# Kernel tuning notes

Measured on AMD Instinct MI355X. Metric: run time of the kernel, lower is better.

Reference implementation:

```python
import jax, jax.numpy as jnp
import numpy as np

T, N = 1024, 128
V, H, VS, KS = 35, 512, 128, 128
MAX_LEN = 250


def setup_inputs() -> dict:
    key = jax.random.key(0)
    ks = jax.random.split(key, 16)
    s = 0.05
    emb = jax.random.normal(ks[0], (V, H), jnp.float32) * s
    emb = emb.at[0].set(0.0)  # padding_idx=0
    return {
        'enc_key': jax.random.normal(ks[1], (T, N, KS), jnp.float32),
        'enc_value': jax.random.normal(ks[2], (T, N, VS), jnp.float32),
        'lens': jax.random.randint(ks[3], (N,), 1, T, jnp.int32),
        'emb': emb,
        'W_ih1': jax.random.normal(ks[4], (4 * H, H + VS), jnp.float32) * s,
        'W_hh1': jax.random.normal(ks[5], (4 * H, H), jnp.float32) * s,
        'b_ih1': jax.random.normal(ks[6], (4 * H,), jnp.float32) * s,
        'b_hh1': jax.random.normal(ks[7], (4 * H,), jnp.float32) * s,
        'W_ih2': jax.random.normal(ks[8], (4 * KS, H), jnp.float32) * s,
        'W_hh2': jax.random.normal(ks[9], (4 * KS, KS), jnp.float32) * s,
        'b_ih2': jax.random.normal(ks[10], (4 * KS,), jnp.float32) * s,
        'b_hh2': jax.random.normal(ks[11], (4 * KS,), jnp.float32) * s,
        'W_out': jax.random.normal(ks[12], (V, KS + VS), jnp.float32) * s,
        'b_out': jax.random.normal(ks[13], (V,), jnp.float32) * s,
    }


def _lstm_cell(x, h, c, W_ih, W_hh, b_ih, b_hh):
    # PyTorch LSTMCell gate order: i, f, g, o
    g = x @ W_ih.T + b_ih + h @ W_hh.T + b_hh
    i, f, gg, o = jnp.split(g, 4, axis=-1)
    c_new = jax.nn.sigmoid(f) * c + jax.nn.sigmoid(i) * jnp.tanh(gg)
    h_new = jax.nn.sigmoid(o) * jnp.tanh(c_new)
    return h_new, c_new


def reference(enc_key, enc_value, lens, emb, W_ih1, W_hh1, b_ih1, b_hh1,
              W_ih2, W_hh2, b_ih2, b_hh2, W_out, b_out):
    # eval-mode forward (isTrain=False): greedy decode for MAX_LEN steps.
    key_t = jnp.transpose(enc_key, (1, 0, 2))    # (N, T, KS)
    val_t = jnp.transpose(enc_value, (1, 0, 2))  # (N, T, VS)
    values_mean = enc_value.mean(axis=0)         # (N, VS) -- fed to lstm1 every step (as in source)
    mask = jnp.arange(T)[None, :] >= lens[:, None]  # (N, T) True = masked

    h1 = jnp.zeros((N, H), enc_key.dtype)
    c1 = jnp.zeros((N, H), enc_key.dtype)
    h2 = jnp.zeros((N, KS), enc_key.dtype)
    c2 = jnp.zeros((N, KS), enc_key.dtype)
    tok0 = jnp.zeros((N,), jnp.int32)  # argmax of ones(N,1)*33 over size-1 dim == 0

    def step(carry, _):
        h1, c1, h2, c2, tok = carry
        char_embed = emb[tok]                                  # (N, H)
        inp = jnp.concatenate([char_embed, values_mean], axis=1)
        h1n, c1n = _lstm_cell(inp, h1, c1, W_ih1, W_hh1, b_ih1, b_hh1)
        h2n, c2n = _lstm_cell(h1n, h2, c2, W_ih2, W_hh2, b_ih2, b_hh2)
        energy = jnp.einsum('ntk,nk->nt', key_t, h2n)          # (N, T)
        energy = jnp.where(mask, -1e9, energy)
        attn = jax.nn.softmax(energy, axis=1)
        ctx = jnp.einsum('nt,ntv->nv', attn, val_t)            # (N, VS)
        pred = jnp.concatenate([h2n, ctx], axis=1) @ W_out.T + b_out  # (N, V)
        tok_n = jnp.argmax(pred, axis=-1).astype(jnp.int32)
        return (h1n, c1n, h2n, c2n, tok_n), pred

    _, preds = jax.lax.scan(step, (h1, c1, h2, c2, tok0), None, length=MAX_LEN)
    return jnp.transpose(preds, (1, 0, 2))  # (N, MAX_LEN, V)
```

## Files before the change

### kernel.cpp

```cpp
#include <hip/hip_runtime.h>
#include <math.h>

typedef unsigned int u32;
typedef unsigned long long ull;
typedef float f4v __attribute__((ext_vector_type(4)));

#define T_     1024
#define N_     128
#define V_     35
#define H_     512
#define VS_    128
#define KS_    128
#define MAXLEN 250
#define NBLK   256

#define OFF_TOKF   0
#define OFF_H1F    512
#define OFF_H2OF   1536
#define OFF_H2HF   2048
#define OFF_PFLAG  2560
#define OFF_PMS    3072
#define OFF_H2P    4096
#define OFF_PCTX   69632
#define OFF_VM     135168
#define OFF_EMBG   200704
#define OFF_VMG    487424
#define OFF_H1A    1536000
#define OFF_H1B    1798144
#define OFF_W1P    2060288
#define OFF_W2TO   6254592
#define OFF_W2TH   6909952
#define OFF_B2O    7565312
#define OFF_B2H    7566336
#define OFF_WO2    7567360
#define OFF_KT     8388608ull
#define OFF_VT     75497472ull
#define WS_T_NEED  142606336ull

#define ASF_STR 516
#define WSBUF   4352

__device__ __forceinline__ float sigf(float x){ return 1.0f/(1.0f+expf(-x)); }
__device__ __forceinline__ float dot4(float4 a, float4 b){ return a.x*b.x + a.y*b.y + a.z*b.z + a.w*b.w; }

__device__ __forceinline__ float cohloadf(const float* p){
  return __hip_atomic_load(p, __ATOMIC_RELAXED, __HIP_MEMORY_SCOPE_AGENT);
}
__device__ __forceinline__ void cohstoref(float* p, float v){
  __hip_atomic_store(p, v, __ATOMIC_RELAXED, __HIP_MEMORY_SCOPE_AGENT);
}
__device__ __forceinline__ ull cohloadu(const ull* p){
  return __hip_atomic_load(p, __ATOMIC_RELAXED, __HIP_MEMORY_SCOPE_AGENT);
}
__device__ __forceinline__ u32 cohloadw(const u32* p){
  return __hip_atomic_load(p, __ATOMIC_RELAXED, __HIP_MEMORY_SCOPE_AGENT);
}
__device__ __forceinline__ void cohstorew(u32* p, u32 v){
  __hip_atomic_store(p, v, __ATOMIC_RELAXED, __HIP_MEMORY_SCOPE_AGENT);
}

__global__ void prep_state(const float* __restrict__ val, char* __restrict__ ws){
  __shared__ float part[256];
  float* vmarr = (float*)(ws + OFF_VM);
  float* h1A   = (float*)(ws + OFF_H1A);
  const int n = blockIdx.x, tid = threadIdx.x;
  const int c = tid >> 7, v = tid & 127;
  float acc = 0.f;
  const float* vp = val + (size_t)(c*512)*N_*VS_ + (size_t)n*VS_ + v;
  #pragma unroll 8
  for (int t = 0; t < 512; ++t) acc += vp[(size_t)t*N_*VS_];
  part[tid] = acc;
  __syncthreads();
  if (tid < 128) vmarr[(size_t)n*128 + tid] = (part[tid] + part[tid+128]) * (1.0f/1024.0f);
  h1A[(size_t)n*H_ + tid]       = 0.f;
  h1A[(size_t)n*H_ + 256 + tid] = 0.f;
}

__global__ void prep_embG(const float* __restrict__ emb, const float* __restrict__ W_ih1,
                          char* __restrict__ ws){
  float* embG = (float*)(ws + OFF_EMBG);
  const int v = blockIdx.x >> 3, cb = blockIdx.x & 7;
  const int c = cb*256 + threadIdx.x;
  const int row_w = (c & 3)*H_ + (c >> 2);
  const float4* w4 = (const float4*)(W_ih1 + (size_t)row_w*640);
  const float4* e4 = (const float4*)(emb + (size_t)v*H_);
  float s = 0.f;
  #pragma unroll 8
  for (int k = 0; k < 128; ++k) s += dot4(w4[k], e4[k]);
  embG[(size_t)v*2048 + c] = s;
}

__global__ void prep_vmG(const float* __restrict__ W_ih1, const float* __restrict__ b_ih1,
                         const float* __restrict__ b_hh1, char* __restrict__ ws){
  float* vmG = (float*)(ws + OFF_VMG);
  const float* vmarr = (const float*)(ws + OFF_VM);
  const int n = blockIdx.x >> 3, cb = blockIdx.x & 7;
  const int c = cb*256 + threadIdx.x;
  const int row_w = (c & 3)*H_ + (c >> 2);
  const float4* w4 = (const float4*)(W_ih1 + (size_t)row_w*640 + 512);
  const float4* v4 = (const float4*)(vmarr + (size_t)n*128);
  float s = b_ih1[row_w] + b_hh1[row_w];
  #pragma unroll 8
  for (int k = 0; k < 32; ++k) s += dot4(w4[k], v4[k]);
  vmG[(size_t)n*2048 + c] = s;
}

__global__ void prep_W1p(const float* __restrict__ W_hh1, char* __restrict__ ws){
  float* Wp1 = (float*)(ws + OFF_W1P);
  const int ct = blockIdx.x >> 3, ch = blockIdx.x & 7, tid = threadIdx.x;
  const int c_st = tid >> 2, seg = tid & 3;
  const int sgl = ct*64 + c_st, row_w = (sgl & 3)*H_ + (sgl >> 2);
  const float* src = W_hh1 + (size_t)row_w*H_ + ch*64 + seg*16;
  float* dstb = Wp1 + (size_t)ct*32768 + ch*4096 + tid*4;
  #pragma unroll
  for (int j = 0; j < 4; ++j)
    *(float4*)(dstb + j*1024) = *(const float4*)(src + j*4);
}

__global__ void prep_W2T(const float* __restrict__ W_ih2, const float* __restrict__ W_hh2,
                         const float* __restrict__ b_ih2, const float* __restrict__ b_hh2,
                         char* __restrict__ ws){
  float* W2To = (float*)(ws + OFF_W2TO);
  float* W2Th = (float*)(ws + OFF_W2TH);
  const int k = blockIdx.x, tid = threadIdx.x;
  const int g = tid >> 6, uu = tid & 63;
  const int rowO = g*128 + uu, rowH = g*128 + 64 + uu;
  float vo, vh;
  if (k < 512){ vo = W_ih2[(size_t)rowO*512 + k]; vh = W_ih2[(size_t)rowH*512 + k]; }
  else        { vo = W_hh2[(size_t)rowO*128 + (k-512)]; vh = W_hh2[(size_t)rowH*128 + (k-512)]; }
  W2To[(size_t)k*256 + tid] = vo;
  W2Th[(size_t)k*256 + tid] = vh;
  if (k == 0){
    ((float*)(ws + OFF_B2O))[tid] = b_ih2[rowO] + b_hh2[rowO];
    ((float*)(ws + OFF_B2H))[tid] = b_ih2[rowH] + b_hh2[rowH];
  }
}

__global__ void prep_Wo2(const float* __restrict__ W_out, char* __restrict__ ws){
  float* Wo2 = (float*)(ws + OFF_WO2);
  const int idx = blockIdx.x*256 + threadIdx.x;
  const int k = idx >> 6, v = idx & 63;
  Wo2[idx] = (v < V_) ? W_out[(size_t)v*256 + k] : 0.f;
}

__global__ void prep_transpose(const float* __restrict__ key, const float* __restrict__ val,
                               char* __restrict__ ws){
  float* keyT = (float*)(ws + OFF_KT);
  float* valT = (float*)(ws + OFF_VT);
  const int bt = blockIdx.x & 1023;
  const bool isv = blockIdx.x >= 1024;
  const float* src = isv ? val : key;
  float* dst = isv ? valT : keyT;
  const int nn = threadIdx.x >> 1, hf = threadIdx.x & 1;
  const float4* s4 = (const float4*)(src + ((size_t)bt*N_ + nn)*KS_ + hf*64);
  float4* d4 = (float4*)(dst + ((size_t)nn*T_ + bt)*KS_ + hf*64);
  #pragma unroll
  for (int i = 0; i < 16; ++i) d4[i] = s4[i];
}

__global__ __launch_bounds__(256, 1) void decoder_main(
  const float* __restrict__ keyA, const float* __restrict__ valA,
  const ull nstr, const ull kstr,
  const int* __restrict__ lens, const float* __restrict__ b_out,
  float* __restrict__ out, char* __restrict__ ws)
{
  __shared__ __align__(16) float smem[16*ASF_STR + 2*WSBUF];
  __shared__ float c1_keep[256];
  __shared__ float h2_keep[128];
  __shared__ float c2_keep[64];
  __shared__ int   toksh[16];

  float* AsF = smem;
  float* WsB = smem + 16*ASF_STR;

  u32* tokflag = (u32*)(ws + OFF_TOKF);
  u32* h1flag  = (u32*)(ws + OFF_H1F);
  u32* h2of    = (u32*)(ws + OFF_H2OF);
  u32* h2hf    = (u32*)(ws + OFF_H2HF);
  u32* pflag   = (u32*)(ws + OFF_PFLAG);
  float* pms   = (float*)(ws + OFF_PMS);
  float* h2p   = (float*)(ws + OFF_H2P);
  float* pctx  = (float*)(ws + OFF_PCTX);
  float* embG  = (float*)(ws + OFF_EMBG);
  float* vmG   = (float*)(ws + OFF_VMG);
  float* h1cur = (float*)(ws + OFF_H1A);
  float* h1nxt = (float*)(ws + OFF_H1B);
  const float* Wp1 = (const float*)(ws + OFF_W1P);
  const float* Wo2 = (const float*)(ws + OFF_WO2);

  const int b = blockIdx.x, tid = threadIdx.x;

  c1_keep[tid] = 0.f;
  if (tid < 128) h2_keep[tid] = 0.f;
  if (tid < 64)  c2_keep[tid] = 0.f;

  const int rt = b >> 5, ct = b & 31;
  const int row0 = rt*16, c0 = ct*64;
  const int lane = tid & 63, qw = tid >> 6;
  const int r_g = lane >> 4, c_g = lane & 15;
  const int c_st = tid >> 2, seg = tid & 3;
  const float* wct = Wp1 + (size_t)ct*32768 + (tid << 2);

  const int n = b & 127;
  const bool owner = (b < 128);
  const float* W2T = (const float*)(ws + (owner ? OFF_W2TO : OFF_W2TH));
  const float* b2  = (const float*)(ws + (owner ? OFF_B2O : OFF_B2H));
  const int len = lens[n];
  const int mid = (7*len) >> 4;
  const int lo = owner ? 0 : mid;
  const int hi = owner ? mid : len;
  const float* krow = keyA + (size_t)n*nstr;
  const float* vrow = valA + (size_t)n*nstr;

  float* xs   = smem;
  float* ctxL = smem + 640;
  float* G2p  = smem + 640;
  float* G2   = smem + 1664;
  float* h2s  = smem + 1920;
  float* Es   = smem + 2048;
  float* red  = smem + 3072;
  float* Cs   = smem + 3136;
  float* Zs   = smem + 4160;
  float* Prp  = smem + 4416;

  #pragma unroll 1
  for (int step = 0; step < MAXLEN; ++step){
    {
      float4 w0 = *(const float4*)(wct),
             w1 = *(const float4*)(wct+1024),
             w2 = *(const float4*)(wct+2048),
             w3 = *(const float4*)(wct+3072);

      if (tid < 16){
        u32 tv;
        const u32 tgt = (u32)step << 8;
        while ((tv = cohloadw(&tokflag[row0 + tid])) < tgt) __builtin_amdgcn_s_sleep(1);
        toksh[tid] = (int)(tv & 255u);
      }
      __syncthreads();

      {
        const ull* src = (const ull*)(h1cur + (size_t)row0*H_);
        ull* dstb = (ull*)AsF;
        #pragma unroll
        for (int i = 0; i < 16; ++i){
          const int u = tid + i*256;
          const int r = u >> 8, cc = u & 255;
          dstb[(size_t)r*258 + cc] = cohloadu(src + u);
        }
      }

      float acc[4][4];
      #pragma unroll
      for (int i = 0; i < 4; ++i){ acc[i][0]=0.f; acc[i][1]=0.f; acc[i][2]=0.f; acc[i][3]=0.f; }

      #pragma unroll 1
      for (int ch = 0; ch < 8; ++ch){
        float* W = WsB + (ch & 1)*WSBUF;
        { float* wd = W + c_st*68 + seg*16;
          ((float4*)wd)[0]=w0; ((float4*)wd)[1]=w1; ((float4*)wd)[2]=w2; ((float4*)wd)[3]=w3;
        }
        if (ch < 7){
          const float* q = wct + (ch+1)*4096;
          w0 = *(const float4*)(q);      w1 = *(const float4*)(q+1024);
          w2 = *(const float4*)(q+2048); w3 = *(const float4*)(q+3072);
        }
        __syncthreads();
        const int kbase = ch*64;
        #pragma unroll
        for (int kq = 0; kq < 4; ++kq){
          const int t4 = (qw*4 + kq)*4;
          float4 wv0 = *(const float4*)(W + (c_g   )*68 + t4);
          float4 wv1 = *(const float4*)(W + (c_g+16)*68 + t4);
          float4 wv2 = *(const float4*)(W + (c_g+32)*68 + t4);
          float4 wv3 = *(const float4*)(W + (c_g+48)*68 + t4);
          const int ko = kbase + t4;
          float4 av0 = *(const float4*)(AsF + (r_g   )*ASF_STR + ko);
          float4 av1 = *(const float4*)(AsF + (r_g+ 4)*ASF_STR + ko);
          float4 av2 = *(const float4*)(AsF + (r_g+ 8)*ASF_STR + ko);
          float4 av3 = *(const float4*)(AsF + (r_g+12)*ASF_STR + ko);
          acc[0][0]+=dot4(av0,wv0); acc[0][1]+=dot4(av0,wv1); acc[0][2]+=dot4(av0,wv2); acc[0][3]+=dot4(av0,wv3);
          acc[1][0]+=dot4(av1,wv0); acc[1][1]+=dot4(av1,wv1); acc[1][2]+=dot4(av1,wv2); acc[1][3]+=dot4(av1,wv3);
          acc[2][0]+=dot4(av2,wv0); acc[2][1]+=dot4(av2,wv1); acc[2][2]+=dot4(av2,wv2); acc[2][3]+=dot4(av2,wv3);
          acc[3][0]+=dot4(av3,wv0); acc[3][1]+=dot4(av3,wv1); acc[3][2]+=dot4(av3,wv2); acc[3][3]+=dot4(av3,wv3);
        }
        __syncthreads();
      }
      float* Red = WsB;
      #pragma unroll
      for (int ri = 0; ri < 4; ++ri)
        #pragma unroll
        for (int ci = 0; ci < 4; ++ci)
          Red[((ri*4+ci)*4 + qw)*64 + lane] = acc[ri][ci];
      __syncthreads();
      float* Gs = AsF;
      { const int l2 = tid & 63, g = tid >> 6;
        const int row_l = (l2 >> 4) + 4*g;
        const int nrow = row0 + row_l;
        const float* eg = embG + (size_t)toksh[row_l]*2048 + c0;
        const float* vg = vmG  + (size_t)nrow*2048 + c0;
        #pragma unroll
        for (int j = 0; j < 4; ++j){
          const int a = g*4 + j;
          const float* rp = Red + a*256 + l2;
          float s = rp[0] + rp[64] + rp[128] + rp[192];
          const int col_l = (l2 & 15) + 16*j;
          s += eg[col_l] + vg[col_l];
          Gs[row_l*68 + col_l] = s;
        }
      }
      __syncthreads();
      { const int r = tid >> 4, hl = tid & 15;
        float4 q = *(const float4*)(Gs + r*68 + hl*4);
        const int row = row0 + r, hid = ct*16 + hl;
        float cold = c1_keep[tid];
        float cn = sigf(q.y)*cold + sigf(q.x)*tanhf(q.z);
        float hn = sigf(q.w)*tanhf(cn);
        c1_keep[tid] = cn;
        cohstoref(h1nxt + (size_t)row*H_ + hid, hn);
      }
      __syncthreads();
      if (tid == 0) cohstorew(&h1flag[rt*32 + ct], (u32)(step+1));
    }

    {
      if (tid < 32){
        while (cohloadw(&h1flag[(n >> 4)*32 + tid]) < (u32)(step+1)) __builtin_amdgcn_s_sleep(1);
      }
      __syncthreads();
      xs[tid]       = cohloadf(h1nxt + (size_t)n*H_ + tid);
      xs[256 + tid] = cohloadf(h1nxt + (size_t)n*H_ + 256 + tid);
      if (tid < 128) xs[512 + tid] = h2_keep[tid];
      __syncthreads();

      {
        const int kw = tid >> 6, cl = tid & 63;
        const float* Wt = W2T + (size_t)kw*160*256 + cl*4;
        const float* xk = xs + kw*160;
        f4v acc = {0.f,0.f,0.f,0.f};
        #pragma unroll 4
        for (int k = 0; k < 160; ++k)
          acc += xk[k] * *(const f4v*)(Wt + (size_t)k*256);
        ((f4v*)(G2p + kw*256))[cl] = acc;
      }
      __syncthreads();
      G2[tid] = G2p[tid] + G2p[256+tid] + G2p[512+tid] + G2p[768+tid] + b2[tid];
      __syncthreads();
      if (tid < 64){
        const int unit = owner ? tid : (64 + tid);
        float gi = G2[tid], gf = G2[64+tid], gg = G2[128+tid], go = G2[192+tid];
        float cold = c2_keep[tid];
        float cn = sigf(gf)*cold + sigf(gi)*tanhf(gg);
        float hn = sigf(go)*tanhf(cn);
        c2_keep[tid] = cn;
        cohstoref(h2p + (size_t)n*128 + unit, hn);
      }
      __syncthreads();
      if (tid == 0){
        cohstorew(owner ? &h2of[n] : &h2hf[n], (u32)(step+1));
        u32* of = owner ? &h2hf[n] : &h2of[n];
        while (cohloadw(of) < (u32)(step+1)) __builtin_amdgcn_s_sleep(1);
      }
      __syncthreads();
      if (tid < 128){
        float hv = cohloadf(h2p + (size_t)n*128 + tid);
        h2s[tid] = hv; h2_keep[tid] = hv;
      }
      __syncthreads();
    }

    {
      const float4* h2f = (const float4*)h2s;
      const int grp = tid >> 4, gj = tid & 15;
      const float4 hq0 = h2f[gj*2], hq1 = h2f[gj*2+1];
      for (int t = lo + grp; t < hi; t += 16){
        const float4* kp = (const float4*)(krow + (size_t)t*kstr + gj*8);
        float e = dot4(kp[0], hq0) + dot4(kp[1], hq1);
        e += __shfl_xor(e, 1); e += __shfl_xor(e, 2);
        e += __shfl_xor(e, 4); e += __shfl_xor(e, 8);
        if (gj == 0) Es[t] = e;
      }
      __syncthreads();
      float lm = -3.0e38f;
      for (int t = lo + tid; t < hi; t += 256) lm = fmaxf(lm, Es[t]);
      #pragma unroll
      for (int off = 32; off > 0; off >>= 1) lm = fmaxf(lm, __shfl_xor(lm, off));
      if (lane == 0) red[qw] = lm;
      __syncthreads();
      const float m_l = fmaxf(fmaxf(red[0], red[1]), fmaxf(red[2], red[3]));
      __syncthreads();
      float ls = 0.f;
      for (int t = lo + tid; t < hi; t += 256){ float p = expf(Es[t]-m_l); Es[t] = p; ls += p; }
      #pragma unroll
      for (int off = 32; off > 0; off >>= 1) ls += __shfl_xor(ls, off);
      if (lane == 0) red[qw] = ls;
      __syncthreads();
      const float s_l = red[0] + red[1] + red[2] + red[3];
      { const int part = tid >> 5, v4i = (tid & 31)*4;
        f4v a0 = {0.f,0.f,0.f,0.f}, a1 = a0, a2 = a0, a3 = a0;
        int t = lo + part;
        for (; t + 24 < hi; t += 32){
          float p0 = Es[t], p1 = Es[t+8], p2 = Es[t+16], p3 = Es[t+24];
          f4v u0 = *(const f4v*)(vrow + (size_t)(t    )*kstr + v4i);
          f4v u1 = *(const f4v*)(vrow + (size_t)(t+ 8 )*kstr + v4i);
          f4v u2 = *(const f4v*)(vrow + (size_t)(t+16 )*kstr + v4i);
          f4v u3 = *(const f4v*)(vrow + (size_t)(t+24 )*kstr + v4i);
          a0 += p0*u0; a1 += p1*u1; a2 += p2*u2; a3 += p3*u3;
        }
        for (; t < hi; t += 8){
          f4v u0 = *(const f4v*)(vrow + (size_t)t*kstr + v4i);
          a0 += Es[t]*u0;
        }
        f4v ctv = a0 + a1 + a2 + a3;
        Cs[part*128 + v4i+0]=ctv.x; Cs[part*128 + v4i+1]=ctv.y;
        Cs[part*128 + v4i+2]=ctv.z; Cs[part*128 + v4i+3]=ctv.w;
      }
      __syncthreads();
      if (tid < 128){
        float s = 0.f;
        #pragma unroll
        for (int p8 = 0; p8 < 8; ++p8) s += Cs[p8*128 + tid];
        ctxL[tid] = s;
      }
      __syncthreads();

      if (!owner){
        if (tid < 128) cohstoref(pctx + (size_t)n*128 + tid, ctxL[tid]);
        if (tid == 0){ cohstoref(pms + 2*n, m_l); cohstoref(pms + 2*n + 1, s_l); }
        __syncthreads();
        if (tid == 0) cohstorew(&pflag[n], (u32)(step+1));
      } else {
        if (tid == 0){
          while (cohloadw(&pflag[n]) < (u32)(step+1)) __builtin_amdgcn_s_sleep(1);
        }
        __syncthreads();
        if (tid < 128){
          float m2 = cohloadf(pms + 2*n), s2v = cohloadf(pms + 2*n + 1);
          float c2v = cohloadf(pctx + (size_t)n*128 + tid);
          float m = fmaxf(m_l, m2);
          float e1 = expf(m_l - m), e2 = expf(m2 - m);
          float denom = e1*s_l + e2*s2v;
          Zs[tid]       = h2s[tid];
          Zs[128 + tid] = (e1*ctxL[tid] + e2*c2v) / denom;
        }
        __syncthreads();
        {
          const int kw = tid >> 6, lv = tid & 63;
          const float* wp = Wo2 + (size_t)kw*64*64 + lv;
          const float* zk = Zs + kw*64;
          float a = 0.f;
          #pragma unroll 8
          for (int k = 0; k < 64; ++k) a += zk[k]*wp[(size_t)k*64];
          Prp[kw*64 + lv] = a;
        }
        __syncthreads();
        if (tid < 64){
          float s = Prp[tid] + Prp[64+tid] + Prp[128+tid] + Prp[192+tid];
          float av = (tid < V_) ? (s + b_out[tid]) : -3.0e38f;
          if (tid < V_) out[((size_t)n*MAXLEN + step)*V_ + tid] = av;
          float bv = av; int bi = tid;
          #pragma unroll
          for (int off = 32; off > 0; off >>= 1){
            float ov = __shfl_xor(bv, off);
            int   oi = __shfl_xor(bi, off);
            if (ov > bv || (ov == bv && oi < bi)){ bv = ov; bi = oi; }
          }
          if (tid == 0) cohstorew(&tokflag[n], ((u32)(step+1) << 8) | (u32)bi);
        }
      }
    }
    __syncthreads();
    float* tp = h1cur; h1cur = h1nxt; h1nxt = tp;
  }
}

extern "C" void kernel_launch(void* const* d_in, const int* in_sizes, int n_in,
                              void* d_out, int out_size, void* d_ws, size_t ws_size,
                              hipStream_t stream)
{
  const float* key    = (const float*)d_in[0];
  const float* val    = (const float*)d_in[1];
  const int*   lens   = (const int*)d_in[2];
  const float* emb    = (const float*)d_in[3];
  const float* W_ih1  = (const float*)d_in[4];
  const float* W_hh1  = (const float*)d_in[5];
  const float* b_ih1  = (const float*)d_in[6];
  const float* b_hh1  = (const float*)d_in[7];
  const float* W_ih2  = (const float*)d_in[8];
  const float* W_hh2  = (const float*)d_in[9];
  const float* b_ih2  = (const float*)d_in[10];
  const float* b_hh2  = (const float*)d_in[11];
  const float* W_out  = (const float*)d_in[12];
  const float* b_out  = (const float*)d_in[13];

  (void)in_sizes; (void)n_in; (void)out_size;

  (void)hipMemsetAsync(d_ws, 0, 4096, stream);
  prep_state<<<128, 256, 0, stream>>>(val, (char*)d_ws);
  prep_embG<<<280, 256, 0, stream>>>(emb, W_ih1, (char*)d_ws);
  prep_vmG<<<1024, 256, 0, stream>>>(W_ih1, b_ih1, b_hh1, (char*)d_ws);
  prep_W1p<<<256, 256, 0, stream>>>(W_hh1, (char*)d_ws);
  prep_W2T<<<640, 256, 0, stream>>>(W_ih2, W_hh2, b_ih2, b_hh2, (char*)d_ws);
  prep_Wo2<<<64, 256, 0, stream>>>(W_out, (char*)d_ws);

  const int use_t = (ws_size >= WS_T_NEED) ? 1 : 0;
  const float* keyA = key; const float* valA = val;
  ull nstr = (ull)KS_, kstr = (ull)N_*KS_;
  if (use_t){
    prep_transpose<<<2048, 256, 0, stream>>>(key, val, (char*)d_ws);
    keyA = (const float*)((char*)d_ws + OFF_KT);
    valA = (const float*)((char*)d_ws + OFF_VT);
    nstr = (ull)T_*KS_; kstr = (ull)KS_;
  }

  decoder_main<<<NBLK, 256, 0, stream>>>(
      keyA, valA, nstr, kstr, lens, b_out,
      (float*)d_out, (char*)d_ws);
}
```

Before: 14.41 ms.

## Split attention over four blocks per sequence when occupancy allows two blocks per CU

When the occupancy query reports at least two resident blocks per CU, the persistent decoder launches 512 blocks instead of 256. Each sequence's time axis is then split into four chunks: 256 extra blocks handle only attention and wait on the h2 flags. The owner block merges three partial softmax/context results instead of one, and the energy loop is unrolled by two. The aim is to spread the memory-bound key/value attention across more CUs and shorten each step's critical path. The cost is more flag polling and merge work, and the spin-wait scheme only works if all 512 blocks are actually co-resident.

```diff
diff --git a/kernel.cpp b/kernel.cpp
--- a/kernel.cpp
+++ b/kernel.cpp
@@ -12,27 +12,26 @@
 #define VS_    128
 #define KS_    128
 #define MAXLEN 250
-#define NBLK   256
 
 #define OFF_TOKF   0
 #define OFF_H1F    512
 #define OFF_H2OF   1536
 #define OFF_H2HF   2048
 #define OFF_PFLAG  2560
-#define OFF_PMS    3072
-#define OFF_H2P    4096
-#define OFF_PCTX   69632
-#define OFF_VM     135168
-#define OFF_EMBG   200704
-#define OFF_VMG    487424
-#define OFF_H1A    1536000
-#define OFF_H1B    1798144
-#define OFF_W1P    2060288
-#define OFF_W2TO   6254592
-#define OFF_W2TH   6909952
-#define OFF_B2O    7565312
-#define OFF_B2H    7566336
-#define OFF_WO2    7567360
+#define OFF_PMS    4096
+#define OFF_H2P    8192
+#define OFF_PCTX   73728
+#define OFF_VM     270336
+#define OFF_EMBG   335872
+#define OFF_VMG    622592
+#define OFF_H1A    1671168
+#define OFF_H1B    1933312
+#define OFF_W1P    2195456
+#define OFF_W2TO   6389760
+#define OFF_W2TH   7045120
+#define OFF_B2O    7700480
+#define OFF_B2H    7701504
+#define OFF_WO2    7702528
 #define OFF_KT     8388608ull
 #define OFF_VT     75497472ull
 #define WS_T_NEED  142606336ull
@@ -160,7 +159,7 @@
 
 __global__ __launch_bounds__(256, 1) void decoder_main(
   const float* __restrict__ keyA, const float* __restrict__ valA,
-  const ull nstr, const ull kstr,
+  const ull nstr, const ull kstr, const int nsplit,
   const int* __restrict__ lens, const float* __restrict__ b_out,
   float* __restrict__ out, char* __restrict__ ws)
 {
@@ -189,26 +188,35 @@
   const float* Wo2 = (const float*)(ws + OFF_WO2);
 
   const int b = blockIdx.x, tid = threadIdx.x;
+  const int roleIdx = b >> 7;
+  const int n = b & 127;
+  const bool owner = (roleIdx == 0);
+  const bool isAB  = (b < 256);
 
   c1_keep[tid] = 0.f;
   if (tid < 128) h2_keep[tid] = 0.f;
   if (tid < 64)  c2_keep[tid] = 0.f;
 
   const int rt = b >> 5, ct = b & 31;
-  const int row0 = rt*16, c0 = ct*64;
+  const int row0 = (rt & 7)*16, c0 = ct*64;
   const int lane = tid & 63, qw = tid >> 6;
   const int r_g = lane >> 4, c_g = lane & 15;
   const int c_st = tid >> 2, seg = tid & 3;
   const float* wct = Wp1 + (size_t)ct*32768 + (tid << 2);
 
-  const int n = b & 127;
-  const bool owner = (b < 128);
   const float* W2T = (const float*)(ws + (owner ? OFF_W2TO : OFF_W2TH));
   const float* b2  = (const float*)(ws + (owner ? OFF_B2O : OFF_B2H));
   const int len = lens[n];
-  const int mid = (7*len) >> 4;
-  const int lo = owner ? 0 : mid;
-  const int hi = owner ? mid : len;
+  int w0i, w1i;
+  if (nsplit == 4){
+    w0i = (roleIdx==0) ? 0 : (roleIdx==1) ? 6 : (roleIdx==2) ? 15 : 24;
+    w1i = (roleIdx==0) ? 6 : (roleIdx==1) ? 15 : (roleIdx==2) ? 24 : 32;
+  } else {
+    w0i = (roleIdx==0) ? 0 : 14;
+    w1i = (roleIdx==0) ? 14 : 32;
+  }
+  const int lo = (len*w0i) >> 5;
+  const int hi = (len*w1i) >> 5;
   const float* krow = keyA + (size_t)n*nstr;
   const float* vrow = valA + (size_t)n*nstr;
 
@@ -225,7 +233,7 @@
 
   #pragma unroll 1
   for (int step = 0; step < MAXLEN; ++step){
-    {
+    if (isAB){
       float4 w0 = *(const float4*)(wct),
              w1 = *(const float4*)(wct+1024),
              w2 = *(const float4*)(wct+2048),
@@ -320,10 +328,10 @@
         cohstoref(h1nxt + (size_t)row*H_ + hid, hn);
       }
       __syncthreads();
-      if (tid == 0) cohstorew(&h1flag[rt*32 + ct], (u32)(step+1));
+      if (tid == 0) cohstorew(&h1flag[(rt & 7)*32 + ct], (u32)(step+1));
     }
 
-    {
+    if (isAB){
       if (tid < 32){
         while (cohloadw(&h1flag[(n >> 4)*32 + tid]) < (u32)(step+1)) __builtin_amdgcn_s_sleep(1);
       }
@@ -367,13 +375,34 @@
         h2s[tid] = hv; h2_keep[tid] = hv;
       }
       __syncthreads();
+    } else {
+      if (tid == 0){
+        while (cohloadw(&h2of[n]) < (u32)(step+1)) __builtin_amdgcn_s_sleep(1);
+        while (cohloadw(&h2hf[n]) < (u32)(step+1)) __builtin_amdgcn_s_sleep(1);
+      }
+      __syncthreads();
+      if (tid < 128) h2s[tid] = cohloadf(h2p + (size_t)n*128 + tid);
+      __syncthreads();
     }
 
     {
       const float4* h2f = (const float4*)h2s;
       const int grp = tid >> 4, gj = tid & 15;
       const float4 hq0 = h2f[gj*2], hq1 = h2f[gj*2+1];
-      for (int t = lo + grp; t < hi; t += 16){
+      int t = lo + grp;
+      for (; t + 16 < hi; t += 32){
+        const float4* kp0 = (const float4*)(krow + (size_t)t*kstr + gj*8);
+        const float4* kp1 = (const float4*)(krow + (size_t)(t+16)*kstr + gj*8);
+        float4 a0 = kp0[0], a1 = kp0[1], b0v = kp1[0], b1v = kp1[1];
+        float e0 = dot4(a0,hq0) + dot4(a1,hq1);
+        float e1 = dot4(b0v,hq0) + dot4(b1v,hq1);
+        e0 += __shfl_xor(e0, 1); e1 += __shfl_xor(e1, 1);
+        e0 += __shfl_xor(e0, 2); e1 += __shfl_xor(e1, 2);
+        e0 += __shfl_xor(e0, 4); e1 += __shfl_xor(e1, 4);
+        e0 += __shfl_xor(e0, 8); e1 += __shfl_xor(e1, 8);
+        if (gj == 0){ Es[t] = e0; Es[t+16] = e1; }
+      }
+      for (; t < hi; t += 16){
         const float4* kp = (const float4*)(krow + (size_t)t*kstr + gj*8);
         float e = dot4(kp[0], hq0) + dot4(kp[1], hq1);
         e += __shfl_xor(e, 1); e += __shfl_xor(e, 2);
@@ -382,7 +411,7 @@
       }
       __syncthreads();
       float lm = -3.0e38f;
-      for (int t = lo + tid; t < hi; t += 256) lm = fmaxf(lm, Es[t]);
+      for (int tt = lo + tid; tt < hi; tt += 256) lm = fmaxf(lm, Es[tt]);
       #pragma unroll
       for (int off = 32; off > 0; off >>= 1) lm = fmaxf(lm, __shfl_xor(lm, off));
       if (lane == 0) red[qw] = lm;
@@ -390,7 +419,7 @@
       const float m_l = fmaxf(fmaxf(red[0], red[1]), fmaxf(red[2], red[3]));
       __syncthreads();
       float ls = 0.f;
-      for (int t = lo + tid; t < hi; t += 256){ float p = expf(Es[t]-m_l); Es[t] = p; ls += p; }
+      for (int tt = lo + tid; tt < hi; tt += 256){ float p = expf(Es[tt]-m_l); Es[tt] = p; ls += p; }
       #pragma unroll
       for (int off = 32; off > 0; off >>= 1) ls += __shfl_xor(ls, off);
       if (lane == 0) red[qw] = ls;
@@ -398,18 +427,18 @@
       const float s_l = red[0] + red[1] + red[2] + red[3];
       { const int part = tid >> 5, v4i = (tid & 31)*4;
         f4v a0 = {0.f,0.f,0.f,0.f}, a1 = a0, a2 = a0, a3 = a0;
-        int t = lo + part;
-        for (; t + 24 < hi; t += 32){
-          float p0 = Es[t], p1 = Es[t+8], p2 = Es[t+16], p3 = Es[t+24];
-          f4v u0 = *(const f4v*)(vrow + (size_t)(t    )*kstr + v4i);
-          f4v u1 = *(const f4v*)(vrow + (size_t)(t+ 8 )*kstr + v4i);
-          f4v u2 = *(const f4v*)(vrow + (size_t)(t+16 )*kstr + v4i);
-          f4v u3 = *(const f4v*)(vrow + (size_t)(t+24 )*kstr + v4i);
+        int tc = lo + part;
+        for (; tc + 24 < hi; tc += 32){
+          float p0 = Es[tc], p1 = Es[tc+8], p2 = Es[tc+16], p3 = Es[tc+24];
+          f4v u0 = *(const f4v*)(vrow + (size_t)(tc    )*kstr + v4i);
+          f4v u1 = *(const f4v*)(vrow + (size_t)(tc+ 8 )*kstr + v4i);
+          f4v u2 = *(const f4v*)(vrow + (size_t)(tc+16 )*kstr + v4i);
+          f4v u3 = *(const f4v*)(vrow + (size_t)(tc+24 )*kstr + v4i);
           a0 += p0*u0; a1 += p1*u1; a2 += p2*u2; a3 += p3*u3;
         }
-        for (; t < hi; t += 8){
-          f4v u0 = *(const f4v*)(vrow + (size_t)t*kstr + v4i);
-          a0 += Es[t]*u0;
+        for (; tc < hi; tc += 8){
+          f4v u0 = *(const f4v*)(vrow + (size_t)tc*kstr + v4i);
+          a0 += Es[tc]*u0;
         }
         f4v ctv = a0 + a1 + a2 + a3;
         Cs[part*128 + v4i+0]=ctv.x; Cs[part*128 + v4i+1]=ctv.y;
@@ -424,24 +453,35 @@
       }
       __syncthreads();
 
-      if (!owner){
-        if (tid < 128) cohstoref(pctx + (size_t)n*128 + tid, ctxL[tid]);
-        if (tid == 0){ cohstoref(pms + 2*n, m_l); cohstoref(pms + 2*n + 1, s_l); }
+      if (roleIdx != 0){
+        const int hs = roleIdx - 1;
+        if (tid < 128) cohstoref(pctx + (size_t)hs*16384 + (size_t)n*128 + tid, ctxL[tid]);
+        if (tid == 0){ cohstoref(pms + hs*256 + 2*n, m_l); cohstoref(pms + hs*256 + 2*n + 1, s_l); }
         __syncthreads();
-        if (tid == 0) cohstorew(&pflag[n], (u32)(step+1));
+        if (tid == 0) cohstorew(&pflag[hs*128 + n], (u32)(step+1));
       } else {
         if (tid == 0){
-          while (cohloadw(&pflag[n]) < (u32)(step+1)) __builtin_amdgcn_s_sleep(1);
+          for (int hs = 0; hs < nsplit-1; ++hs){
+            while (cohloadw(&pflag[hs*128 + n]) < (u32)(step+1)) __builtin_amdgcn_s_sleep(1);
+          }
         }
         __syncthreads();
         if (tid < 128){
-          float m2 = cohloadf(pms + 2*n), s2v = cohloadf(pms + 2*n + 1);
-          float c2v = cohloadf(pctx + (size_t)n*128 + tid);
-          float m = fmaxf(m_l, m2);
-          float e1 = expf(m_l - m), e2 = expf(m2 - m);
-          float denom = e1*s_l + e2*s2v;
+          float m = m_l;
+          for (int hs = 0; hs < nsplit-1; ++hs)
+            m = fmaxf(m, cohloadf(pms + hs*256 + 2*n));
+          float e0 = expf(m_l - m);
+          float denom = e0*s_l;
+          float cacc  = e0*ctxL[tid];
+          for (int hs = 0; hs < nsplit-1; ++hs){
+            float mh = cohloadf(pms + hs*256 + 2*n);
+            float sh = cohloadf(pms + hs*256 + 2*n + 1);
+            float ch = cohloadf(pctx + (size_t)hs*16384 + (size_t)n*128 + tid);
+            float e = expf(mh - m);
+            denom += e*sh; cacc += e*ch;
+          }
           Zs[tid]       = h2s[tid];
-          Zs[128 + tid] = (e1*ctxL[tid] + e2*c2v) / denom;
+          Zs[128 + tid] = cacc / denom;
         }
         __syncthreads();
         {
@@ -495,7 +535,7 @@
 
   (void)in_sizes; (void)n_in; (void)out_size;
 
-  (void)hipMemsetAsync(d_ws, 0, 4096, stream);
+  (void)hipMemsetAsync(d_ws, 0, 8192, stream);
   prep_state<<<128, 256, 0, stream>>>(val, (char*)d_ws);
   prep_embG<<<280, 256, 0, stream>>>(emb, W_ih1, (char*)d_ws);
   prep_vmG<<<1024, 256, 0, stream>>>(W_ih1, b_ih1, b_hh1, (char*)d_ws);
@@ -513,7 +553,12 @@
     nstr = (ull)T_*KS_; kstr = (ull)KS_;
   }
 
-  decoder_main<<<NBLK, 256, 0, stream>>>(
-      keyA, valA, nstr, kstr, lens, b_out,
+  int maxb = 0;
+  (void)hipOccupancyMaxActiveBlocksPerMultiprocessor(&maxb, decoder_main, 256, 0);
+  const int nsplit = (maxb >= 2) ? 4 : 2;
+  const int grid   = (nsplit == 4) ? 512 : 256;
+
+  decoder_main<<<grid, 256, 0, stream>>>(
+      keyA, valA, nstr, kstr, nsplit, lens, b_out,
       (float*)d_out, (char*)d_ws);
 }
```

Result: faster. 12.61 ms (-12.5%).

## Add helper prefetch blocks that warm key/value rows into cache each step

Applied to the files above, without the earlier changes.

Launches an extra 256 blocks when occupancy allows two blocks per CU. The helper blocks spin on the per-sequence token flag and then stream that sequence's key and value rows, keeping them resident in cache (L2/MALL) for the attention pass of the compute blocks. Workspace offsets are shifted to make room, and the host queries device and function attributes to decide the grid size. The helpers add memory traffic and contend for CU resources. If co-residency does not hold, they rely on a bounded spin to avoid deadlock.

```diff
diff --git a/kernel.cpp b/kernel.cpp
--- a/kernel.cpp
+++ b/kernel.cpp
@@ -1,5 +1,6 @@
 #include <hip/hip_runtime.h>
 #include <math.h>
+#include <string.h>
 
 typedef unsigned int u32;
 typedef unsigned long long ull;
@@ -12,27 +13,26 @@
 #define VS_    128
 #define KS_    128
 #define MAXLEN 250
-#define NBLK   256
 
 #define OFF_TOKF   0
 #define OFF_H1F    512
 #define OFF_H2OF   1536
 #define OFF_H2HF   2048
 #define OFF_PFLAG  2560
-#define OFF_PMS    3072
-#define OFF_H2P    4096
-#define OFF_PCTX   69632
-#define OFF_VM     135168
-#define OFF_EMBG   200704
-#define OFF_VMG    487424
-#define OFF_H1A    1536000
-#define OFF_H1B    1798144
-#define OFF_W1P    2060288
-#define OFF_W2TO   6254592
-#define OFF_W2TH   6909952
-#define OFF_B2O    7565312
-#define OFF_B2H    7566336
-#define OFF_WO2    7567360
+#define OFF_PMS    4096
+#define OFF_H2P    8192
+#define OFF_PCTX   73728
+#define OFF_VM     270336
+#define OFF_EMBG   335872
+#define OFF_VMG    622592
+#define OFF_H1A    1671168
+#define OFF_H1B    1933312
+#define OFF_W1P    2195456
+#define OFF_W2TO   6389760
+#define OFF_W2TH   7045120
+#define OFF_B2O    7700480
+#define OFF_B2H    7701504
+#define OFF_WO2    7702528
 #define OFF_KT     8388608ull
 #define OFF_VT     75497472ull
 #define WS_T_NEED  142606336ull
@@ -170,10 +170,45 @@
   __shared__ float c2_keep[64];
   __shared__ int   toksh[16];
 
+  u32* tokflag = (u32*)(ws + OFF_TOKF);
+
+  const int b = blockIdx.x, tid = threadIdx.x;
+
+  if (b >= 256){
+    const int n2   = b & 127;
+    const int half = ((b >> 7) == 2) ? 0 : 1;
+    const int len2 = lens[n2];
+    const int mid2 = (7*len2) >> 4;
+    const int plo  = half ? mid2 : 0;
+    const int phi  = half ? len2 : mid2;
+    const float* kr = keyA + (size_t)n2*nstr;
+    const float* vr = valA + (size_t)n2*nstr;
+    const int rown = tid >> 3;
+    const int segi = (tid & 7) * 4;
+    f4v sink = {0.f,0.f,0.f,0.f};
+    for (int step = 0; step < MAXLEN; ++step){
+      const u32 tgt = (u32)step << 8;
+      int sp = 0;
+      while (cohloadw(&tokflag[n2]) < tgt){
+        __builtin_amdgcn_s_sleep(16);
+        if (++sp > (1<<19)) break;
+      }
+      for (int t = plo + rown; t < phi; t += 32){
+        const f4v* kp = (const f4v*)(kr + (size_t)t*kstr) + segi;
+        sink += kp[0]; sink += kp[1]; sink += kp[2]; sink += kp[3];
+      }
+      for (int t = plo + rown; t < phi; t += 32){
+        const f4v* vp = (const f4v*)(vr + (size_t)t*kstr) + segi;
+        sink += vp[0]; sink += vp[1]; sink += vp[2]; sink += vp[3];
+      }
+    }
+    asm volatile("" :: "v"(sink[0]), "v"(sink[1]), "v"(sink[2]), "v"(sink[3]));
+    return;
+  }
+
   float* AsF = smem;
   float* WsB = smem + 16*ASF_STR;
 
-  u32* tokflag = (u32*)(ws + OFF_TOKF);
   u32* h1flag  = (u32*)(ws + OFF_H1F);
   u32* h2of    = (u32*)(ws + OFF_H2OF);
   u32* h2hf    = (u32*)(ws + OFF_H2HF);
@@ -187,8 +222,6 @@
   float* h1nxt = (float*)(ws + OFF_H1B);
   const float* Wp1 = (const float*)(ws + OFF_W1P);
   const float* Wo2 = (const float*)(ws + OFF_WO2);
-
-  const int b = blockIdx.x, tid = threadIdx.x;
 
   c1_keep[tid] = 0.f;
   if (tid < 128) h2_keep[tid] = 0.f;
@@ -382,7 +415,7 @@
       }
       __syncthreads();
       float lm = -3.0e38f;
-      for (int t = lo + tid; t < hi; t += 256) lm = fmaxf(lm, Es[t]);
+      for (int tt = lo + tid; tt < hi; tt += 256) lm = fmaxf(lm, Es[tt]);
       #pragma unroll
       for (int off = 32; off > 0; off >>= 1) lm = fmaxf(lm, __shfl_xor(lm, off));
       if (lane == 0) red[qw] = lm;
@@ -390,7 +423,7 @@
       const float m_l = fmaxf(fmaxf(red[0], red[1]), fmaxf(red[2], red[3]));
       __syncthreads();
       float ls = 0.f;
-      for (int t = lo + tid; t < hi; t += 256){ float p = expf(Es[t]-m_l); Es[t] = p; ls += p; }
+      for (int tt = lo + tid; tt < hi; tt += 256){ float p = expf(Es[tt]-m_l); Es[tt] = p; ls += p; }
       #pragma unroll
       for (int off = 32; off > 0; off >>= 1) ls += __shfl_xor(ls, off);
       if (lane == 0) red[qw] = ls;
@@ -398,18 +431,18 @@
       const float s_l = red[0] + red[1] + red[2] + red[3];
       { const int part = tid >> 5, v4i = (tid & 31)*4;
         f4v a0 = {0.f,0.f,0.f,0.f}, a1 = a0, a2 = a0, a3 = a0;
-        int t = lo + part;
-        for (; t + 24 < hi; t += 32){
-          float p0 = Es[t], p1 = Es[t+8], p2 = Es[t+16], p3 = Es[t+24];
-          f4v u0 = *(const f4v*)(vrow + (size_t)(t    )*kstr + v4i);
-          f4v u1 = *(const f4v*)(vrow + (size_t)(t+ 8 )*kstr + v4i);
-          f4v u2 = *(const f4v*)(vrow + (size_t)(t+16 )*kstr + v4i);
-          f4v u3 = *(const f4v*)(vrow + (size_t)(t+24 )*kstr + v4i);
+        int tc = lo + part;
+        for (; tc + 24 < hi; tc += 32){
+          float p0 = Es[tc], p1 = Es[tc+8], p2 = Es[tc+16], p3 = Es[tc+24];
+          f4v u0 = *(const f4v*)(vrow + (size_t)(tc    )*kstr + v4i);
+          f4v u1 = *(const f4v*)(vrow + (size_t)(tc+ 8 )*kstr + v4i);
+          f4v u2 = *(const f4v*)(vrow + (size_t)(tc+16 )*kstr + v4i);
+          f4v u3 = *(const f4v*)(vrow + (size_t)(tc+24 )*kstr + v4i);
           a0 += p0*u0; a1 += p1*u1; a2 += p2*u2; a3 += p3*u3;
         }
-        for (; t < hi; t += 8){
-          f4v u0 = *(const f4v*)(vrow + (size_t)t*kstr + v4i);
-          a0 += Es[t]*u0;
+        for (; tc < hi; tc += 8){
+          f4v u0 = *(const f4v*)(vrow + (size_t)tc*kstr + v4i);
+          a0 += Es[tc]*u0;
         }
         f4v ctv = a0 + a1 + a2 + a3;
         Cs[part*128 + v4i+0]=ctv.x; Cs[part*128 + v4i+1]=ctv.y;
@@ -495,7 +528,7 @@
 
   (void)in_sizes; (void)n_in; (void)out_size;
 
-  (void)hipMemsetAsync(d_ws, 0, 4096, stream);
+  (void)hipMemsetAsync(d_ws, 0, 8192, stream);
   prep_state<<<128, 256, 0, stream>>>(val, (char*)d_ws);
   prep_embG<<<280, 256, 0, stream>>>(emb, W_ih1, (char*)d_ws);
   prep_vmG<<<1024, 256, 0, stream>>>(W_ih1, b_ih1, b_hh1, (char*)d_ws);
@@ -513,7 +546,26 @@
     nstr = (ull)T_*KS_; kstr = (ull)KS_;
   }
 
-  decoder_main<<<NBLK, 256, 0, stream>>>(
+  int dev = 0; (void)hipGetDevice(&dev);
+  hipDeviceProp_t prop; memset(&prop, 0, sizeof(prop));
+  (void)hipGetDeviceProperties(&prop, dev);
+  hipFuncAttributes fa; memset(&fa, 0, sizeof(fa));
+  (void)hipFuncGetAttributes(&fa, reinterpret_cast<const void*>(decoder_main));
+  size_t lds_cu = prop.sharedMemPerMultiprocessor;
+  if (prop.gcnArchName[0] && strstr(prop.gcnArchName, "gfx950") && lds_cu < 160*1024)
+    lds_cu = 160*1024;
+  int maxb_hw = 0;
+  if (fa.sharedSizeBytes > 0) maxb_hw = (int)(lds_cu / fa.sharedSizeBytes);
+  if (fa.numRegs > 0 && prop.regsPerBlock > 0){
+    int maxb_reg = prop.regsPerBlock / (256 * fa.numRegs);
+    if (maxb_reg < maxb_hw) maxb_hw = maxb_reg;
+  }
+  int maxb_api = 0;
+  (void)hipOccupancyMaxActiveBlocksPerMultiprocessor(&maxb_api, decoder_main, 256, 0);
+  const int maxb = (maxb_hw > maxb_api) ? maxb_hw : maxb_api;
+  const int grid = (maxb >= 2) ? 512 : 256;
+
+  decoder_main<<<grid, 256, 0, stream>>>(
       keyA, valA, nstr, kstr, lens, b_out,
       (float*)d_out, (char*)d_ws);
 }
```

New measurement: 14.31 ms. Within noise of the previous version (-0.7%).
